# Performance work log

Measured on AMD Instinct MI355X. Metric: run time of the kernel, lower is better.

Reference implementation:

```python
import jax, jax.numpy as jnp
import numpy as np

ALPHA = 0.2  # LeakyReLU negative slope

def setup_inputs() -> dict:
    key = jax.random.key(0)
    k1, k2 = jax.random.split(key)
    K, N = 4096, 1024
    x = jax.random.normal(k1, (K, N), dtype=jnp.float32)
    # xavier_uniform with gain 1.414 on shape (2N, 1)
    limit = 1.414 * np.sqrt(6.0 / (2 * N + 1))
    w = jax.random.uniform(k2, (2 * N, 1), dtype=jnp.float32, minval=-limit, maxval=limit)
    return {"x": x, "w": w}

def reference(x, w):
    # Faithful to: e[i,j] = leakyrelu(concat(x[i], x[j]) @ w)
    # Split w into halves -> outer-sum score (same math, no KxK x 2N intermediate).
    N = x.shape[1]
    w1 = w[:N, 0]   # (N,)
    w2 = w[N:, 0]   # (N,)
    s1 = x @ w1     # (K,)
    s2 = x @ w2     # (K,)
    e = jax.nn.leaky_relu(s1[:, None] + s2[None, :], negative_slope=ALPHA)  # (K, K)
    attention = jax.nn.softmax(e, axis=1)  # dropout p=0.0 -> identity
    h = attention @ x  # (K, N)
    return h
```

## Files before the change

kernel.cpp:

```cpp
#include <hip/hip_runtime.h>

#define KDIM 4096
#define NDIM 1024
#define ALPHA 0.2f
#define LOG2E 1.4426950408889634f
#define CCH 256
#define RCH 16
#define PFL 256

__device__ __align__(16) float g_s1L[KDIM];
__device__ __align__(16) float g_s2L[KDIM];
__device__ __align__(16) float g_E [2 * KDIM];
__device__ __align__(16) float g_F1[KDIM];
__device__ __align__(16) float g_F2[KDIM];
__device__ __align__(16) int   g_t  [KDIM];
__device__ __align__(16) int   g_sig[KDIM];
__device__ __align__(16) float g_cs [CCH][2 * NDIM];
__device__ __align__(16) float g_pre[CCH][2 * NDIM];
__device__ __align__(16) float g_tot[2 * NDIM];
__device__ __align__(16) float g_cz [2 * CCH];
__device__ __align__(16) float g_zpre[2 * CCH];
__device__ __align__(16) float g_ztot[2];

__global__ __launch_bounds__(256) void k_dots(const float* __restrict__ x,
                                              const float* __restrict__ w){
  const int wid = threadIdx.x >> 6, lane = threadIdx.x & 63;
  const int row = blockIdx.x * 4 + wid;
  const float* xr = x + (size_t)row * NDIM;
  float d1 = 0.f, d2 = 0.f;
  #pragma unroll
  for (int q = 0; q < 4; ++q){
    const int off = q * 256 + lane * 4;
    float4 X  = *(const float4*)(xr + off);
    float4 W1 = *(const float4*)(w + off);
    float4 W2 = *(const float4*)(w + NDIM + off);
    d1 = fmaf(X.x, W1.x, fmaf(X.y, W1.y, fmaf(X.z, W1.z, fmaf(X.w, W1.w, d1))));
    d2 = fmaf(X.x, W2.x, fmaf(X.y, W2.y, fmaf(X.z, W2.z, fmaf(X.w, W2.w, d2))));
  }
  #pragma unroll
  for (int m = 32; m >= 1; m >>= 1){
    d1 += __shfl_xor(d1, m, 64);
    d2 += __shfl_xor(d2, m, 64);
  }
  if (lane == 0){
    const float s1 = d1 * LOG2E, s2 = d2 * LOG2E;
    g_s1L[row] = s1;
    g_s2L[row] = s2;
    g_E[2 * row]     = __builtin_amdgcn_exp2f(s2);
    g_E[2 * row + 1] = __builtin_amdgcn_exp2f(ALPHA * s2);
    g_F1[row] = __builtin_amdgcn_exp2f(s1);
    g_F2[row] = __builtin_amdgcn_exp2f(ALPHA * s1);
  }
}

__global__ __launch_bounds__(256) void k_rank(){
  __shared__ __align__(16) float s2s[KDIM];
  const int tid = threadIdx.x;
  #pragma unroll
  for (int q = 0; q < 4; ++q)
    ((float4*)s2s)[q * 256 + tid] = ((const float4*)g_s2L)[q * 256 + tid];
  __syncthreads();
  const int grp = tid >> 4, sub = tid & 15;
  const int o = blockIdx.x * 16 + grp;
  int cnt = 0;
  if (o < KDIM){
    const float val = s2s[o];
    #pragma unroll 4
    for (int m = 0; m < 64; ++m){
      const int q4 = m * 16 + sub;
      const float4 v = ((const float4*)s2s)[q4];
      const int j0 = q4 * 4;
      cnt += (v.x > val || (v.x == val && (j0    ) < o));
      cnt += (v.y > val || (v.y == val && (j0 + 1) < o));
      cnt += (v.z > val || (v.z == val && (j0 + 2) < o));
      cnt += (v.w > val || (v.w == val && (j0 + 3) < o));
    }
  } else {
    const float thr = -g_s1L[o - KDIM];
    #pragma unroll 4
    for (int m = 0; m < 64; ++m){
      const int q4 = m * 16 + sub;
      const float4 v = ((const float4*)s2s)[q4];
      cnt += (v.x >= thr) + (v.y >= thr) + (v.z >= thr) + (v.w >= thr);
    }
  }
  cnt += __shfl_xor(cnt, 1, 64); cnt += __shfl_xor(cnt, 2, 64);
  cnt += __shfl_xor(cnt, 4, 64); cnt += __shfl_xor(cnt, 8, 64);
  if (sub == 0){
    if (o < KDIM) g_sig[cnt] = o;
    else          g_t[o - KDIM] = cnt;
  }
}

__global__ __launch_bounds__(256) void k_chunksum(const float* __restrict__ x){
  __shared__ int   js [RCH];
  __shared__ float e1s[RCH], e2s[RCH];
  const int c = blockIdx.x, tid = threadIdx.x;
  if (tid < RCH){
    const int j = g_sig[c * RCH + tid];
    js[tid]  = j;
    e1s[tid] = g_E[2 * j];
    e2s[tid] = g_E[2 * j + 1];
  }
  __syncthreads();
  if (tid == 0){
    float a = 0.f, b = 0.f;
    #pragma unroll
    for (int r = 0; r < RCH; ++r){ a += e1s[r]; b += e2s[r]; }
    g_cz[2 * c] = a; g_cz[2 * c + 1] = b;
  }
  float4 a1 = {0.f, 0.f, 0.f, 0.f}, a2 = {0.f, 0.f, 0.f, 0.f};
  #pragma unroll
  for (int r = 0; r < RCH; ++r){
    const float4 xv = *(const float4*)(x + (size_t)js[r] * NDIM + tid * 4);
    const float e1 = e1s[r], e2 = e2s[r];
    a1.x = fmaf(e1, xv.x, a1.x); a1.y = fmaf(e1, xv.y, a1.y);
    a1.z = fmaf(e1, xv.z, a1.z); a1.w = fmaf(e1, xv.w, a1.w);
    a2.x = fmaf(e2, xv.x, a2.x); a2.y = fmaf(e2, xv.y, a2.y);
    a2.z = fmaf(e2, xv.z, a2.z); a2.w = fmaf(e2, xv.w, a2.w);
  }
  *(float4*)&g_cs[c][tid * 4]        = a1;
  *(float4*)&g_cs[c][NDIM + tid * 4] = a2;
}

__global__ __launch_bounds__(256) void k_chunkscan(){
  __shared__ float TL[CCH][32];
  __shared__ float SS[8][32];
  const int tid = threadIdx.x;
  const int s = tid >> 5, k = tid & 31;
  const int col = blockIdx.x * 32 + k;
  float run = 0.f;
  #pragma unroll 8
  for (int m = 0; m < 32; ++m){
    const float v = g_cs[s * 32 + m][col];
    TL[s * 32 + m][k] = v;
    run += v;
  }
  SS[s][k] = run;
  __syncthreads();
  if (s == 0){
    float acc = 0.f;
    #pragma unroll
    for (int t = 0; t < 8; ++t){
      const float v = SS[t][k];
      SS[t][k] = acc;
      acc += v;
    }
    g_tot[col] = acc;
  }
  __syncthreads();
  run = SS[s][k];
  #pragma unroll 8
  for (int m = 0; m < 32; ++m){
    g_pre[s * 32 + m][col] = run;
    run += TL[s * 32 + m][k];
  }
  if (blockIdx.x == 0 && tid < 64){
    float v1[4], v2[4];
    #pragma unroll
    for (int q = 0; q < 4; ++q){
      v1[q] = g_cz[2 * (tid * 4 + q)];
      v2[q] = g_cz[2 * (tid * 4 + q) + 1];
    }
    const float s1 = v1[0] + v1[1] + v1[2] + v1[3];
    const float s2 = v2[0] + v2[1] + v2[2] + v2[3];
    float i1 = s1, i2 = s2;
    #pragma unroll
    for (int d = 1; d < 64; d <<= 1){
      const float t1 = __shfl_up(i1, d, 64);
      const float t2 = __shfl_up(i2, d, 64);
      if (tid >= d){ i1 += t1; i2 += t2; }
    }
    float e1 = i1 - s1, e2 = i2 - s2;
    #pragma unroll
    for (int q = 0; q < 4; ++q){
      g_zpre[2 * (tid * 4 + q)]     = e1;
      g_zpre[2 * (tid * 4 + q) + 1] = e2;
      e1 += v1[q]; e2 += v2[q];
    }
    if (tid == 63){ g_ztot[0] = e1; g_ztot[1] = e2; }
  }
}

__global__ __launch_bounds__(256) void k_emit(const float* __restrict__ x,
                                              float* __restrict__ out){
  __shared__ int    js [RCH];
  __shared__ float  e1s[RCH], e2s[RCH];
  __shared__ int    cnt[RCH + 1];
  __shared__ int    off[RCH + 2];
  __shared__ int    pos[RCH + 1];
  __shared__ int    ilist[KDIM];
  __shared__ float2 pfl[PFL];
  const int c = blockIdx.x, tid = threadIdx.x;
  const bool last = (c == CCH - 1);
  const int nbuck = last ? RCH + 1 : RCH;
  if (tid < RCH){
    const int j = g_sig[c * RCH + tid];
    js[tid]  = j;
    e1s[tid] = g_E[2 * j];
    e2s[tid] = g_E[2 * j + 1];
  }
  if (tid <= RCH) cnt[tid] = 0;
  __syncthreads();

  const int tbase = c * RCH;
  int myi[16], myr[16];
  #pragma unroll
  for (int q = 0; q < 16; ++q){
    const int i = q * 256 + tid;
    const int t = g_t[i];
    const int r = t - tbase;
    const bool in = (r >= 0) && (r < nbuck);
    myi[q] = i;
    myr[q] = in ? r : -1;
    if (in) atomicAdd(&cnt[r], 1);
  }
  __syncthreads();
  if (tid == 0){
    int run = 0;
    #pragma unroll
    for (int r = 0; r <= RCH; ++r){
      const int v = cnt[r];
      off[r] = run; pos[r] = run;
      run += v;
    }
    off[RCH + 1] = run;
  }
  __syncthreads();
  #pragma unroll
  for (int q = 0; q < 16; ++q){
    if (myr[q] >= 0){
      const int p = atomicAdd(&pos[myr[q]], 1);
      ilist[p] = myi[q];
      if (p < PFL)
        pfl[p] = make_float2(g_F1[myi[q]], g_F2[myi[q]]);
    }
  }
  __syncthreads();

  float4 a1 = *(const float4*)&g_pre[c][tid * 4];
  float4 a2 = *(const float4*)&g_pre[c][NDIM + tid * 4];
  const float4 t2 = *(const float4*)&g_tot[NDIM + tid * 4];
  float za1 = g_zpre[2 * c], za2 = g_zpre[2 * c + 1];
  const float zt2 = g_ztot[1];
  float4 v[RCH];
  #pragma unroll
  for (int r = 0; r < RCH; ++r)
    v[r] = *(const float4*)(x + (size_t)js[r] * NDIM + tid * 4);

  #pragma unroll
  for (int r = 0; r < RCH; ++r){
    for (int e = off[r]; e < off[r + 1]; ++e){
      const int i = ilist[e];
      float F1, F2;
      if (e < PFL){ const float2 pf = pfl[e]; F1 = pf.x; F2 = pf.y; }
      else        { F1 = g_F1[i]; F2 = g_F2[i]; }
      const float rz = 1.0f / fmaf(F1, za1, F2 * (zt2 - za2));
      float4 h;
      h.x = fmaf(F1, a1.x, F2 * (t2.x - a2.x)) * rz;
      h.y = fmaf(F1, a1.y, F2 * (t2.y - a2.y)) * rz;
      h.z = fmaf(F1, a1.z, F2 * (t2.z - a2.z)) * rz;
      h.w = fmaf(F1, a1.w, F2 * (t2.w - a2.w)) * rz;
      *(float4*)(out + (size_t)i * NDIM + tid * 4) = h;
    }
    const float e1 = e1s[r], e2 = e2s[r];
    za1 += e1; za2 += e2;
    const float4 xv = v[r];
    a1.x = fmaf(e1, xv.x, a1.x); a1.y = fmaf(e1, xv.y, a1.y);
    a1.z = fmaf(e1, xv.z, a1.z); a1.w = fmaf(e1, xv.w, a1.w);
    a2.x = fmaf(e2, xv.x, a2.x); a2.y = fmaf(e2, xv.y, a2.y);
    a2.z = fmaf(e2, xv.z, a2.z); a2.w = fmaf(e2, xv.w, a2.w);
  }
  if (last){
    for (int e = off[RCH]; e < off[RCH + 1]; ++e){
      const int i = ilist[e];
      float F1, F2;
      if (e < PFL){ const float2 pf = pfl[e]; F1 = pf.x; F2 = pf.y; }
      else        { F1 = g_F1[i]; F2 = g_F2[i]; }
      const float rz = 1.0f / fmaf(F1, za1, F2 * (zt2 - za2));
      float4 h;
      h.x = fmaf(F1, a1.x, F2 * (t2.x - a2.x)) * rz;
      h.y = fmaf(F1, a1.y, F2 * (t2.y - a2.y)) * rz;
      h.z = fmaf(F1, a1.z, F2 * (t2.z - a2.z)) * rz;
      h.w = fmaf(F1, a1.w, F2 * (t2.w - a2.w)) * rz;
      *(float4*)(out + (size_t)i * NDIM + tid * 4) = h;
    }
  }
}

extern "C" void kernel_launch(void* const* d_in, const int* in_sizes, int n_in,
                              void* d_out, int out_size, void* d_ws, size_t ws_size,
                              hipStream_t stream){
  const float* x = (const float*)d_in[0];
  const float* w = (const float*)d_in[1];
  float* out = (float*)d_out;
  (void)in_sizes; (void)n_in; (void)out_size; (void)d_ws; (void)ws_size;

  k_dots     <<<dim3(1024), dim3(256), 0, stream>>>(x, w);
  k_rank     <<<dim3(512),  dim3(256), 0, stream>>>();
  k_chunksum <<<dim3(CCH),  dim3(256), 0, stream>>>(x);
  k_chunkscan<<<dim3(64),   dim3(256), 0, stream>>>();
  k_emit     <<<dim3(CCH),  dim3(256), 0, stream>>>(x, out);
}
```

Before: 102.6 us.

## Fuse five kernels into one persistent kernel with software grid barriers

```diff
diff --git a/kernel.cpp b/kernel.cpp
--- a/kernel.cpp
+++ b/kernel.cpp
@@ -11,8 +11,7 @@
 __device__ __align__(16) float g_s1L[KDIM];
 __device__ __align__(16) float g_s2L[KDIM];
 __device__ __align__(16) float g_E [2 * KDIM];
-__device__ __align__(16) float g_F1[KDIM];
-__device__ __align__(16) float g_F2[KDIM];
+__device__ __align__(16) float g_F [2 * KDIM];
 __device__ __align__(16) int   g_t  [KDIM];
 __device__ __align__(16) int   g_sig[KDIM];
 __device__ __align__(16) float g_cs [CCH][2 * NDIM];
@@ -21,141 +20,180 @@
 __device__ __align__(16) float g_cz [2 * CCH];
 __device__ __align__(16) float g_zpre[2 * CCH];
 __device__ __align__(16) float g_ztot[2];
-
-__global__ __launch_bounds__(256) void k_dots(const float* __restrict__ x,
-                                              const float* __restrict__ w){
-  const int wid = threadIdx.x >> 6, lane = threadIdx.x & 63;
-  const int row = blockIdx.x * 4 + wid;
-  const float* xr = x + (size_t)row * NDIM;
-  float d1 = 0.f, d2 = 0.f;
-  #pragma unroll
-  for (int q = 0; q < 4; ++q){
-    const int off = q * 256 + lane * 4;
-    float4 X  = *(const float4*)(xr + off);
-    float4 W1 = *(const float4*)(w + off);
-    float4 W2 = *(const float4*)(w + NDIM + off);
-    d1 = fmaf(X.x, W1.x, fmaf(X.y, W1.y, fmaf(X.z, W1.z, fmaf(X.w, W1.w, d1))));
-    d2 = fmaf(X.x, W2.x, fmaf(X.y, W2.y, fmaf(X.z, W2.z, fmaf(X.w, W2.w, d2))));
-  }
-  #pragma unroll
-  for (int m = 32; m >= 1; m >>= 1){
-    d1 += __shfl_xor(d1, m, 64);
-    d2 += __shfl_xor(d2, m, 64);
-  }
-  if (lane == 0){
-    const float s1 = d1 * LOG2E, s2 = d2 * LOG2E;
-    g_s1L[row] = s1;
-    g_s2L[row] = s2;
-    g_E[2 * row]     = __builtin_amdgcn_exp2f(s2);
-    g_E[2 * row + 1] = __builtin_amdgcn_exp2f(ALPHA * s2);
-    g_F1[row] = __builtin_amdgcn_exp2f(s1);
-    g_F2[row] = __builtin_amdgcn_exp2f(ALPHA * s1);
-  }
+__device__ int g_ctr;
+
+__device__ __forceinline__ void gbarrier(int target){
+  __threadfence();
+  __syncthreads();
+  if (threadIdx.x == 0){
+    atomicAdd(&g_ctr, 1);
+    while (atomicAdd(&g_ctr, 0) < target) __builtin_amdgcn_s_sleep(2);
+  }
+  __syncthreads();
+  __threadfence();
 }
 
-__global__ __launch_bounds__(256) void k_rank(){
-  __shared__ __align__(16) float s2s[KDIM];
-  const int tid = threadIdx.x;
-  #pragma unroll
-  for (int q = 0; q < 4; ++q)
-    ((float4*)s2s)[q * 256 + tid] = ((const float4*)g_s2L)[q * 256 + tid];
-  __syncthreads();
-  const int grp = tid >> 4, sub = tid & 15;
-  const int o = blockIdx.x * 16 + grp;
-  int cnt = 0;
-  if (o < KDIM){
-    const float val = s2s[o];
-    #pragma unroll 4
-    for (int m = 0; m < 64; ++m){
-      const int q4 = m * 16 + sub;
-      const float4 v = ((const float4*)s2s)[q4];
-      const int j0 = q4 * 4;
-      cnt += (v.x > val || (v.x == val && (j0    ) < o));
-      cnt += (v.y > val || (v.y == val && (j0 + 1) < o));
-      cnt += (v.z > val || (v.z == val && (j0 + 2) < o));
-      cnt += (v.w > val || (v.w == val && (j0 + 3) < o));
-    }
-  } else {
-    const float thr = -g_s1L[o - KDIM];
-    #pragma unroll 4
-    for (int m = 0; m < 64; ++m){
-      const int q4 = m * 16 + sub;
-      const float4 v = ((const float4*)s2s)[q4];
-      cnt += (v.x >= thr) + (v.y >= thr) + (v.z >= thr) + (v.w >= thr);
-    }
-  }
-  cnt += __shfl_xor(cnt, 1, 64); cnt += __shfl_xor(cnt, 2, 64);
-  cnt += __shfl_xor(cnt, 4, 64); cnt += __shfl_xor(cnt, 8, 64);
-  if (sub == 0){
-    if (o < KDIM) g_sig[cnt] = o;
-    else          g_t[o - KDIM] = cnt;
-  }
-}
-
-__global__ __launch_bounds__(256) void k_chunksum(const float* __restrict__ x){
+__global__ __launch_bounds__(256, 1) void k_all(const float* __restrict__ x,
+                                                const float* __restrict__ w,
+                                                float* __restrict__ out){
+  __shared__ __align__(16) union {
+    float s2s[KDIM];
+    struct { float TL[CCH][32]; float SS[8][32]; } d;
+    struct {
+      int    cnt[RCH + 1], off[RCH + 2], pos[RCH + 1];
+      int    ilist[KDIM];
+      float2 pfl[PFL];
+    } e;
+  } sh;
   __shared__ int   js [RCH];
   __shared__ float e1s[RCH], e2s[RCH];
-  const int c = blockIdx.x, tid = threadIdx.x;
-  if (tid < RCH){
-    const int j = g_sig[c * RCH + tid];
-    js[tid]  = j;
-    e1s[tid] = g_E[2 * j];
-    e2s[tid] = g_E[2 * j + 1];
-  }
-  __syncthreads();
-  if (tid == 0){
-    float a = 0.f, b = 0.f;
-    #pragma unroll
-    for (int r = 0; r < RCH; ++r){ a += e1s[r]; b += e2s[r]; }
-    g_cz[2 * c] = a; g_cz[2 * c + 1] = b;
-  }
-  float4 a1 = {0.f, 0.f, 0.f, 0.f}, a2 = {0.f, 0.f, 0.f, 0.f};
-  #pragma unroll
-  for (int r = 0; r < RCH; ++r){
-    const float4 xv = *(const float4*)(x + (size_t)js[r] * NDIM + tid * 4);
-    const float e1 = e1s[r], e2 = e2s[r];
-    a1.x = fmaf(e1, xv.x, a1.x); a1.y = fmaf(e1, xv.y, a1.y);
-    a1.z = fmaf(e1, xv.z, a1.z); a1.w = fmaf(e1, xv.w, a1.w);
-    a2.x = fmaf(e2, xv.x, a2.x); a2.y = fmaf(e2, xv.y, a2.y);
-    a2.z = fmaf(e2, xv.z, a2.z); a2.w = fmaf(e2, xv.w, a2.w);
-  }
-  *(float4*)&g_cs[c][tid * 4]        = a1;
-  *(float4*)&g_cs[c][NDIM + tid * 4] = a2;
-}
-
-__global__ __launch_bounds__(256) void k_chunkscan(){
-  __shared__ float TL[CCH][32];
-  __shared__ float SS[8][32];
-  const int tid = threadIdx.x;
-  const int s = tid >> 5, k = tid & 31;
-  const int col = blockIdx.x * 32 + k;
-  float run = 0.f;
-  #pragma unroll 8
-  for (int m = 0; m < 32; ++m){
-    const float v = g_cs[s * 32 + m][col];
-    TL[s * 32 + m][k] = v;
-    run += v;
-  }
-  SS[s][k] = run;
-  __syncthreads();
-  if (s == 0){
-    float acc = 0.f;
-    #pragma unroll
-    for (int t = 0; t < 8; ++t){
-      const float v = SS[t][k];
-      SS[t][k] = acc;
-      acc += v;
-    }
-    g_tot[col] = acc;
-  }
-  __syncthreads();
-  run = SS[s][k];
-  #pragma unroll 8
-  for (int m = 0; m < 32; ++m){
-    g_pre[s * 32 + m][col] = run;
-    run += TL[s * 32 + m][k];
-  }
-  if (blockIdx.x == 0 && tid < 64){
+  const int tid = threadIdx.x, lane = tid & 63, wv = tid >> 6;
+  const int bid = blockIdx.x;
+
+  {
+    float4 W1r[4], W2r[4];
+    #pragma unroll
+    for (int q = 0; q < 4; ++q){
+      const int o = q * 256 + lane * 4;
+      W1r[q] = *(const float4*)(w + o);
+      W2r[q] = *(const float4*)(w + NDIM + o);
+    }
+    const int wgid = bid * 4 + wv;
+    #pragma unroll
+    for (int rr = 0; rr < 4; ++rr){
+      const int row = wgid * 4 + rr;
+      const float* xr = x + (size_t)row * NDIM;
+      float d1 = 0.f, d2 = 0.f;
+      #pragma unroll
+      for (int q = 0; q < 4; ++q){
+        const float4 X = *(const float4*)(xr + q * 256 + lane * 4);
+        d1 = fmaf(X.x, W1r[q].x, fmaf(X.y, W1r[q].y, fmaf(X.z, W1r[q].z, fmaf(X.w, W1r[q].w, d1))));
+        d2 = fmaf(X.x, W2r[q].x, fmaf(X.y, W2r[q].y, fmaf(X.z, W2r[q].z, fmaf(X.w, W2r[q].w, d2))));
+      }
+      #pragma unroll
+      for (int m = 32; m >= 1; m >>= 1){
+        d1 += __shfl_xor(d1, m, 64);
+        d2 += __shfl_xor(d2, m, 64);
+      }
+      if (lane == 0){
+        const float s1 = d1 * LOG2E, s2 = d2 * LOG2E;
+        g_s1L[row] = s1;
+        g_s2L[row] = s2;
+        g_E[2 * row]     = __builtin_amdgcn_exp2f(s2);
+        g_E[2 * row + 1] = __builtin_amdgcn_exp2f(ALPHA * s2);
+        g_F[2 * row]     = __builtin_amdgcn_exp2f(s1);
+        g_F[2 * row + 1] = __builtin_amdgcn_exp2f(ALPHA * s1);
+      }
+    }
+  }
+  gbarrier(CCH);
+
+  {
+    #pragma unroll
+    for (int q = 0; q < 4; ++q)
+      ((float4*)sh.s2s)[q * 256 + tid] = ((const float4*)g_s2L)[q * 256 + tid];
+    __syncthreads();
+    const int grp = tid >> 4, sub = tid & 15;
+    #pragma unroll
+    for (int pass = 0; pass < 2; ++pass){
+      const int o = bid * 32 + pass * 16 + grp;
+      int cnt = 0;
+      if (o < KDIM){
+        const float val = sh.s2s[o];
+        #pragma unroll 4
+        for (int m = 0; m < 64; ++m){
+          const int q4 = m * 16 + sub;
+          const float4 v4 = ((const float4*)sh.s2s)[q4];
+          const int j0 = q4 * 4;
+          cnt += (v4.x > val || (v4.x == val && (j0    ) < o));
+          cnt += (v4.y > val || (v4.y == val && (j0 + 1) < o));
+          cnt += (v4.z > val || (v4.z == val && (j0 + 2) < o));
+          cnt += (v4.w > val || (v4.w == val && (j0 + 3) < o));
+        }
+      } else {
+        const float thr = -g_s1L[o - KDIM];
+        #pragma unroll 4
+        for (int m = 0; m < 64; ++m){
+          const int q4 = m * 16 + sub;
+          const float4 v4 = ((const float4*)sh.s2s)[q4];
+          cnt += (v4.x >= thr) + (v4.y >= thr) + (v4.z >= thr) + (v4.w >= thr);
+        }
+      }
+      cnt += __shfl_xor(cnt, 1, 64); cnt += __shfl_xor(cnt, 2, 64);
+      cnt += __shfl_xor(cnt, 4, 64); cnt += __shfl_xor(cnt, 8, 64);
+      if (sub == 0){
+        if (o < KDIM) g_sig[cnt] = o;
+        else          g_t[o - KDIM] = cnt;
+      }
+    }
+  }
+  gbarrier(2 * CCH);
+
+  float4 v[RCH];
+  {
+    const int c = bid;
+    if (tid < RCH){
+      const int j = g_sig[c * RCH + tid];
+      js[tid]  = j;
+      const float2 e = *(const float2*)&g_E[2 * j];
+      e1s[tid] = e.x;
+      e2s[tid] = e.y;
+    }
+    __syncthreads();
+    if (tid == 0){
+      float a = 0.f, b = 0.f;
+      #pragma unroll
+      for (int r = 0; r < RCH; ++r){ a += e1s[r]; b += e2s[r]; }
+      g_cz[2 * c] = a; g_cz[2 * c + 1] = b;
+    }
+    #pragma unroll
+    for (int r = 0; r < RCH; ++r)
+      v[r] = *(const float4*)(x + (size_t)js[r] * NDIM + tid * 4);
+    float4 a1 = {0.f,0.f,0.f,0.f}, a2 = {0.f,0.f,0.f,0.f};
+    #pragma unroll
+    for (int r = 0; r < RCH; ++r){
+      const float e1 = e1s[r], e2 = e2s[r];
+      const float4 xv = v[r];
+      a1.x = fmaf(e1, xv.x, a1.x); a1.y = fmaf(e1, xv.y, a1.y);
+      a1.z = fmaf(e1, xv.z, a1.z); a1.w = fmaf(e1, xv.w, a1.w);
+      a2.x = fmaf(e2, xv.x, a2.x); a2.y = fmaf(e2, xv.y, a2.y);
+      a2.z = fmaf(e2, xv.z, a2.z); a2.w = fmaf(e2, xv.w, a2.w);
+    }
+    *(float4*)&g_cs[c][tid * 4]        = a1;
+    *(float4*)&g_cs[c][NDIM + tid * 4] = a2;
+  }
+  gbarrier(3 * CCH);
+
+  if (bid < 64){
+    const int s = tid >> 5, k2 = tid & 31;
+    const int col = bid * 32 + k2;
+    float run = 0.f;
+    #pragma unroll 8
+    for (int m = 0; m < 32; ++m){
+      const float vv = g_cs[s * 32 + m][col];
+      sh.d.TL[s * 32 + m][k2] = vv;
+      run += vv;
+    }
+    sh.d.SS[s][k2] = run;
+    __syncthreads();
+    if (s == 0){
+      float acc = 0.f;
+      #pragma unroll
+      for (int t = 0; t < 8; ++t){
+        const float vv = sh.d.SS[t][k2];
+        sh.d.SS[t][k2] = acc;
+        acc += vv;
+      }
+      g_tot[col] = acc;
+    }
+    __syncthreads();
+    run = sh.d.SS[s][k2];
+    #pragma unroll 8
+    for (int m = 0; m < 32; ++m){
+      g_pre[s * 32 + m][col] = run;
+      run += sh.d.TL[s * 32 + m][k2];
+    }
+  } else if (bid == 64 && tid < 64){
     float v1[4], v2[4];
     #pragma unroll
     for (int q = 0; q < 4; ++q){
@@ -180,110 +218,91 @@
     }
     if (tid == 63){ g_ztot[0] = e1; g_ztot[1] = e2; }
   }
-}
-
-__global__ __launch_bounds__(256) void k_emit(const float* __restrict__ x,
-                                              float* __restrict__ out){
-  __shared__ int    js [RCH];
-  __shared__ float  e1s[RCH], e2s[RCH];
-  __shared__ int    cnt[RCH + 1];
-  __shared__ int    off[RCH + 2];
-  __shared__ int    pos[RCH + 1];
-  __shared__ int    ilist[KDIM];
-  __shared__ float2 pfl[PFL];
-  const int c = blockIdx.x, tid = threadIdx.x;
-  const bool last = (c == CCH - 1);
-  const int nbuck = last ? RCH + 1 : RCH;
-  if (tid < RCH){
-    const int j = g_sig[c * RCH + tid];
-    js[tid]  = j;
-    e1s[tid] = g_E[2 * j];
-    e2s[tid] = g_E[2 * j + 1];
-  }
-  if (tid <= RCH) cnt[tid] = 0;
-  __syncthreads();
-
-  const int tbase = c * RCH;
-  int myi[16], myr[16];
-  #pragma unroll
-  for (int q = 0; q < 16; ++q){
-    const int i = q * 256 + tid;
-    const int t = g_t[i];
-    const int r = t - tbase;
-    const bool in = (r >= 0) && (r < nbuck);
-    myi[q] = i;
-    myr[q] = in ? r : -1;
-    if (in) atomicAdd(&cnt[r], 1);
-  }
-  __syncthreads();
-  if (tid == 0){
-    int run = 0;
-    #pragma unroll
-    for (int r = 0; r <= RCH; ++r){
-      const int v = cnt[r];
-      off[r] = run; pos[r] = run;
-      run += v;
-    }
-    off[RCH + 1] = run;
-  }
-  __syncthreads();
-  #pragma unroll
-  for (int q = 0; q < 16; ++q){
-    if (myr[q] >= 0){
-      const int p = atomicAdd(&pos[myr[q]], 1);
-      ilist[p] = myi[q];
-      if (p < PFL)
-        pfl[p] = make_float2(g_F1[myi[q]], g_F2[myi[q]]);
-    }
-  }
-  __syncthreads();
-
-  float4 a1 = *(const float4*)&g_pre[c][tid * 4];
-  float4 a2 = *(const float4*)&g_pre[c][NDIM + tid * 4];
-  const float4 t2 = *(const float4*)&g_tot[NDIM + tid * 4];
-  float za1 = g_zpre[2 * c], za2 = g_zpre[2 * c + 1];
-  const float zt2 = g_ztot[1];
-  float4 v[RCH];
-  #pragma unroll
-  for (int r = 0; r < RCH; ++r)
-    v[r] = *(const float4*)(x + (size_t)js[r] * NDIM + tid * 4);
-
-  #pragma unroll
-  for (int r = 0; r < RCH; ++r){
-    for (int e = off[r]; e < off[r + 1]; ++e){
-      const int i = ilist[e];
-      float F1, F2;
-      if (e < PFL){ const float2 pf = pfl[e]; F1 = pf.x; F2 = pf.y; }
-      else        { F1 = g_F1[i]; F2 = g_F2[i]; }
-      const float rz = 1.0f / fmaf(F1, za1, F2 * (zt2 - za2));
-      float4 h;
-      h.x = fmaf(F1, a1.x, F2 * (t2.x - a2.x)) * rz;
-      h.y = fmaf(F1, a1.y, F2 * (t2.y - a2.y)) * rz;
-      h.z = fmaf(F1, a1.z, F2 * (t2.z - a2.z)) * rz;
-      h.w = fmaf(F1, a1.w, F2 * (t2.w - a2.w)) * rz;
-      *(float4*)(out + (size_t)i * NDIM + tid * 4) = h;
-    }
-    const float e1 = e1s[r], e2 = e2s[r];
-    za1 += e1; za2 += e2;
-    const float4 xv = v[r];
-    a1.x = fmaf(e1, xv.x, a1.x); a1.y = fmaf(e1, xv.y, a1.y);
-    a1.z = fmaf(e1, xv.z, a1.z); a1.w = fmaf(e1, xv.w, a1.w);
-    a2.x = fmaf(e2, xv.x, a2.x); a2.y = fmaf(e2, xv.y, a2.y);
-    a2.z = fmaf(e2, xv.z, a2.z); a2.w = fmaf(e2, xv.w, a2.w);
-  }
-  if (last){
-    for (int e = off[RCH]; e < off[RCH + 1]; ++e){
-      const int i = ilist[e];
-      float F1, F2;
-      if (e < PFL){ const float2 pf = pfl[e]; F1 = pf.x; F2 = pf.y; }
-      else        { F1 = g_F1[i]; F2 = g_F2[i]; }
-      const float rz = 1.0f / fmaf(F1, za1, F2 * (zt2 - za2));
-      float4 h;
-      h.x = fmaf(F1, a1.x, F2 * (t2.x - a2.x)) * rz;
-      h.y = fmaf(F1, a1.y, F2 * (t2.y - a2.y)) * rz;
-      h.z = fmaf(F1, a1.z, F2 * (t2.z - a2.z)) * rz;
-      h.w = fmaf(F1, a1.w, F2 * (t2.w - a2.w)) * rz;
-      *(float4*)(out + (size_t)i * NDIM + tid * 4) = h;
+  gbarrier(4 * CCH);
+
+  {
+    const int c = bid;
+    const bool last = (c == CCH - 1);
+    const int nbuck = last ? RCH + 1 : RCH;
+    if (tid <= RCH) sh.e.cnt[tid] = 0;
+    __syncthreads();
+    const int tbase = c * RCH;
+    int myr[16];
+    #pragma unroll
+    for (int q = 0; q < 16; ++q){
+      const int i = q * 256 + tid;
+      const int t = g_t[i];
+      const int r = t - tbase;
+      const bool in = (r >= 0) && (r < nbuck);
+      myr[q] = in ? r : -1;
+      if (in) atomicAdd(&sh.e.cnt[r], 1);
+    }
+    __syncthreads();
+    if (tid == 0){
+      int run = 0;
+      #pragma unroll
+      for (int r = 0; r <= RCH; ++r){
+        const int vv = sh.e.cnt[r];
+        sh.e.off[r] = run; sh.e.pos[r] = run;
+        run += vv;
+      }
+      sh.e.off[RCH + 1] = run;
+    }
+    __syncthreads();
+    #pragma unroll
+    for (int q = 0; q < 16; ++q){
+      if (myr[q] >= 0){
+        const int i = q * 256 + tid;
+        const int p = atomicAdd(&sh.e.pos[myr[q]], 1);
+        sh.e.ilist[p] = i;
+        if (p < PFL) sh.e.pfl[p] = *(const float2*)&g_F[2 * i];
+      }
+    }
+    __syncthreads();
+
+    float4 a1 = *(const float4*)&g_pre[c][tid * 4];
+    float4 a2 = *(const float4*)&g_pre[c][NDIM + tid * 4];
+    const float4 t2 = *(const float4*)&g_tot[NDIM + tid * 4];
+    float za1 = g_zpre[2 * c], za2 = g_zpre[2 * c + 1];
+    const float zt2 = g_ztot[1];
+
+    #pragma unroll
+    for (int r = 0; r < RCH; ++r){
+      for (int e = sh.e.off[r]; e < sh.e.off[r + 1]; ++e){
+        const int i = sh.e.ilist[e];
+        float F1, F2;
+        if (e < PFL){ const float2 pf = sh.e.pfl[e]; F1 = pf.x; F2 = pf.y; }
+        else        { const float2 pf = *(const float2*)&g_F[2 * i]; F1 = pf.x; F2 = pf.y; }
+        const float rz = 1.0f / fmaf(F1, za1, F2 * (zt2 - za2));
+        float4 h;
+        h.x = fmaf(F1, a1.x, F2 * (t2.x - a2.x)) * rz;
+        h.y = fmaf(F1, a1.y, F2 * (t2.y - a2.y)) * rz;
+        h.z = fmaf(F1, a1.z, F2 * (t2.z - a2.z)) * rz;
+        h.w = fmaf(F1, a1.w, F2 * (t2.w - a2.w)) * rz;
+        *(float4*)(out + (size_t)i * NDIM + tid * 4) = h;
+      }
+      const float e1 = e1s[r], e2 = e2s[r];
+      za1 += e1; za2 += e2;
+      const float4 xv = v[r];
+      a1.x = fmaf(e1, xv.x, a1.x); a1.y = fmaf(e1, xv.y, a1.y);
+      a1.z = fmaf(e1, xv.z, a1.z); a1.w = fmaf(e1, xv.w, a1.w);
+      a2.x = fmaf(e2, xv.x, a2.x); a2.y = fmaf(e2, xv.y, a2.y);
+      a2.z = fmaf(e2, xv.z, a2.z); a2.w = fmaf(e2, xv.w, a2.w);
+    }
+    if (last){
+      for (int e = sh.e.off[RCH]; e < sh.e.off[RCH + 1]; ++e){
+        const int i = sh.e.ilist[e];
+        float F1, F2;
+        if (e < PFL){ const float2 pf = sh.e.pfl[e]; F1 = pf.x; F2 = pf.y; }
+        else        { const float2 pf = *(const float2*)&g_F[2 * i]; F1 = pf.x; F2 = pf.y; }
+        const float rz = 1.0f / fmaf(F1, za1, F2 * (zt2 - za2));
+        float4 h;
+        h.x = fmaf(F1, a1.x, F2 * (t2.x - a2.x)) * rz;
+        h.y = fmaf(F1, a1.y, F2 * (t2.y - a2.y)) * rz;
+        h.z = fmaf(F1, a1.z, F2 * (t2.z - a2.z)) * rz;
+        h.w = fmaf(F1, a1.w, F2 * (t2.w - a2.w)) * rz;
+        *(float4*)(out + (size_t)i * NDIM + tid * 4) = h;
+      }
     }
   }
 }
@@ -296,9 +315,8 @@
   float* out = (float*)d_out;
   (void)in_sizes; (void)n_in; (void)out_size; (void)d_ws; (void)ws_size;
 
-  k_dots     <<<dim3(1024), dim3(256), 0, stream>>>(x, w);
-  k_rank     <<<dim3(512),  dim3(256), 0, stream>>>();
-  k_chunksum <<<dim3(CCH),  dim3(256), 0, stream>>>(x);
-  k_chunkscan<<<dim3(64),   dim3(256), 0, stream>>>();
-  k_emit     <<<dim3(CCH),  dim3(256), 0, stream>>>(x, out);
+  static void* ctr_addr = nullptr;
+  if (!ctr_addr) (void)hipGetSymbolAddress(&ctr_addr, HIP_SYMBOL(g_ctr));
+  (void)hipMemsetAsync(ctr_addr, 0, sizeof(int), stream);
+  k_all<<<dim3(256), dim3(256), 0, stream>>>(x, w, out);
 }
```

New measurement: 281.4 us. 174% more time.
